# Performance work log

Hardware: AMD Instinct MI355X
Metric: run time of the kernel (lower is better)

Reference implementation:

```python
import jax, jax.numpy as jnp
import numpy as np
from jax import lax

# ---- config (matches init_kwargs) ----
B, T, H = 4, 2048, 1024
HU = 4 * H                 # h_up = hidden*4
LAYERS, INDEX = 12, 0
K_CLAMP, K_EPS = 60.0, 1e-8
LN_EPS = 1e-5


def setup_inputs() -> dict:
    key = jax.random.key(0)
    ks = jax.random.split(key, 9)
    s = 0.02  # weight scale
    tr01 = INDEX / (LAYERS - 1)          # time_ratio_0_to_1
    tr1pz = 1.0 - INDEX / LAYERS         # time_ratio_1_to_pz
    i_h = np.arange(H, dtype=np.float64) / H
    i_hu = np.arange(HU, dtype=np.float64)
    # per-channel decay speed / first (sized to the WKV channel dim h_up)
    decay_speed = -5.0 + 8.0 * (i_hu / (HU - 1)) ** (0.7 + 1.3 * tr01)
    zigzag = ((np.arange(HU) + 1) % 3 - 1) * 0.5
    time_first = np.log(0.3) + zigzag
    f32 = lambda a: jnp.asarray(a, jnp.float32)
    return {
        "x": jax.random.normal(ks[0], (B, T, H), jnp.float32),
        "ln0_g": jnp.ones((H,), jnp.float32), "ln0_b": jnp.zeros((H,), jnp.float32),
        "pre_g": jnp.ones((H,), jnp.float32), "pre_b": jnp.zeros((H,), jnp.float32),
        "post_g": jnp.ones((H,), jnp.float32), "post_b": jnp.zeros((H,), jnp.float32),
        "tm_decay": f32(decay_speed),
        "tm_first": f32(time_first),
        "tm_mix_k": f32(i_h ** tr1pz),
        "tm_mix_v": f32(i_h ** tr1pz + 0.3 * tr01),
        "tm_mix_r": f32(i_h ** (0.5 * tr1pz)),
        "tm_Wk": jax.random.normal(ks[1], (H, HU), jnp.float32) * s,
        "tm_Wv": jax.random.normal(ks[2], (H, HU), jnp.float32) * s,
        "tm_Wr": jax.random.normal(ks[3], (H, HU), jnp.float32) * s,
        "tm_Wo": jax.random.normal(ks[4], (HU, H), jnp.float32) * s,
        "cm_mix_k": f32(i_h ** tr1pz),
        "cm_mix_r": f32(i_h ** tr1pz),
        "cm_Wk": jax.random.normal(ks[5], (H, HU), jnp.float32) * s,
        "cm_Wv": jax.random.normal(ks[6], (HU, H), jnp.float32) * s,
        "cm_Wr": jax.random.normal(ks[7], (H, H), jnp.float32) * s,
    }


def _ln(x, g, b):
    m = jnp.mean(x, -1, keepdims=True)
    v = jnp.mean((x - m) ** 2, -1, keepdims=True)
    return (x - m) / jnp.sqrt(v + LN_EPS) * g + b


def _shift(x):  # ZeroPad2d((0,0,1,-1)): xx[:, t] = x[:, t-1], xx[:, 0] = 0
    return jnp.pad(x[:, :-1], ((0, 0), (1, 0), (0, 0)))


def _wkv(k, kv, decay, first):
    # k, kv: [B, T, HU]; decay, first: [HU]
    # wkv[t] = first*kv[t] + sum_{d>=1} decay^(d-1) * kv[t-d]  (same for k)
    def step(carry, inp):
        sk, skv = carry
        kt, kvt = inp
        out = (first * kt + sk, first * kvt + skv)
        return (kt + decay * sk, kvt + decay * skv), out
    b = k.shape[0]
    init = (jnp.zeros((b, k.shape[2]), k.dtype), jnp.zeros((b, k.shape[2]), k.dtype))
    _, (wk, wkv) = lax.scan(step, init, (jnp.swapaxes(k, 0, 1), jnp.swapaxes(kv, 0, 1)))
    return jnp.swapaxes(wk, 0, 1), jnp.swapaxes(wkv, 0, 1)


def reference(x, ln0_g, ln0_b, pre_g, pre_b, post_g, post_b,
              tm_decay, tm_first, tm_mix_k, tm_mix_v, tm_mix_r,
              tm_Wk, tm_Wv, tm_Wr, tm_Wo,
              cm_mix_k, cm_mix_r, cm_Wk, cm_Wv, cm_Wr):
    if INDEX == 0:
        x = _ln(x, ln0_g, ln0_b)

    # ---- RWKV_TM (time mix / WKV) ----
    xn = _ln(x, pre_g, pre_b)
    xx = _shift(xn)
    xk = xn * tm_mix_k + xx * (1.0 - tm_mix_k)
    xv = xn * tm_mix_v + xx * (1.0 - tm_mix_v)
    xr = xn * tm_mix_r + xx * (1.0 - tm_mix_r)
    k = jnp.exp(jnp.minimum(xk @ tm_Wk, K_CLAMP))   # [B,T,HU]
    v = xv @ tm_Wv                                  # [B,T,HU]
    r = xr @ tm_Wr                                  # [B,T,HU]
    kv = k * v
    decay = jnp.exp(-jnp.exp(tm_decay))  # per-step multiplier exp(-exp(time_decay))
    first = jnp.exp(tm_first)
    wk, wkv = _wkv(k, kv, decay, first)
    rwkv = jax.nn.sigmoid(r) * (wkv / (wk + K_EPS))
    x = x + rwkv @ tm_Wo

    # ---- RWKV_CM (channel mix) ----
    xn = _ln(x, post_g, post_b)
    xx = _shift(xn)
    xk = xn * cm_mix_k + xx * (1.0 - cm_mix_k)
    xr = xn * cm_mix_r + xx * (1.0 - cm_mix_r)
    kv = jax.nn.silu(xk @ cm_Wk) @ cm_Wv            # [B,T,H]
    x = x + (jax.nn.sigmoid(xr @ cm_Wr) + kv)
    return x
```

## Files before the change

### kernel.cpp

```cpp
#include <hip/hip_runtime.h>

#define Hdim  1024
#define Tdim  2048
#define Bdim  4
#define HUdim 4096
#define Mrows (Bdim*Tdim)
#define CHUNK 2048
#define NCH   (HUdim/CHUNK)
#define NSEG  16
#define SEGL  (Tdim/NSEG)
#define SCHUNK 16

typedef __bf16 bf16;
typedef __bf16 bf16x2 __attribute__((ext_vector_type(2)));
typedef __bf16 bf16x8 __attribute__((ext_vector_type(8)));
typedef float  floatx4 __attribute__((ext_vector_type(4)));

__device__ __forceinline__ bf16 f2bf(float x) { return (bf16)x; }

__global__ __launch_bounds__(256) void wconv_all(
    const float* __restrict__ s0, const float* __restrict__ s1, const float* __restrict__ s2,
    const float* __restrict__ s3, const float* __restrict__ s4, const float* __restrict__ s5,
    const float* __restrict__ s6,
    bf16* d0, bf16* d1, bf16* d2, bf16* d3, bf16* d4, bf16* d5, bf16* d6) {
  __shared__ float tile[64][65];
  int bid = blockIdx.x;
  const float* src; bf16* dst; int K, N, local;
  if (bid < 1024)      { src = s0; dst = d0; K = Hdim;  N = HUdim; local = bid; }
  else if (bid < 2048) { src = s1; dst = d1; K = Hdim;  N = HUdim; local = bid - 1024; }
  else if (bid < 3072) { src = s2; dst = d2; K = Hdim;  N = HUdim; local = bid - 2048; }
  else if (bid < 4096) { src = s3; dst = d3; K = HUdim; N = Hdim;  local = bid - 3072; }
  else if (bid < 5120) { src = s4; dst = d4; K = Hdim;  N = HUdim; local = bid - 4096; }
  else if (bid < 6144) { src = s5; dst = d5; K = HUdim; N = Hdim;  local = bid - 5120; }
  else                 { src = s6; dst = d6; K = Hdim;  N = Hdim;  local = bid - 6144; }
  const int nt = N >> 6;
  const int n0 = (local % nt) * 64, k0 = (local / nt) * 64;
  const int tr = threadIdx.x >> 6;
  const int tc = threadIdx.x & 63;
#pragma unroll
  for (int j = 0; j < 16; j++) {
    int r = j * 4 + tr;
    tile[r][tc] = src[(size_t)(k0 + r) * N + n0 + tc];
  }
  __syncthreads();
#pragma unroll
  for (int j = 0; j < 16; j++) {
    int r = j * 4 + tr;
    dst[(size_t)(n0 + r) * K + k0 + tc] = f2bf(tile[tc][r]);
  }
}

__device__ __forceinline__ void block_reduce4(float v[4], float* sm) {
#pragma unroll
  for (int off = 32; off > 0; off >>= 1) {
#pragma unroll
    for (int i = 0; i < 4; i++) v[i] += __shfl_down(v[i], off, 64);
  }
  const int w = threadIdx.x >> 6;
  if ((threadIdx.x & 63) == 0) {
#pragma unroll
    for (int i = 0; i < 4; i++) sm[w * 4 + i] = v[i];
  }
  __syncthreads();
#pragma unroll
  for (int i = 0; i < 4; i++) v[i] = sm[i] + sm[4 + i] + sm[8 + i] + sm[12 + i];
  __syncthreads();
}

__global__ __launch_bounds__(256) void ln_mix_tm(
    const float* __restrict__ x,
    const float* __restrict__ g0, const float* __restrict__ b0,
    const float* __restrict__ g1, const float* __restrict__ b1,
    const float* __restrict__ mk, const float* __restrict__ mv, const float* __restrict__ mr,
    float* __restrict__ x0, bf16* __restrict__ xk, bf16* __restrict__ xv, bf16* __restrict__ xr) {
  __shared__ float sm[16];
  const int bid = blockIdx.x;
  const int t = bid & (Tdim - 1);
  const int tid = threadIdx.x;
  const bool havep = (t > 0);
  const float hp = havep ? 1.f : 0.f;
  const float* rowc = x + (size_t)bid * Hdim;
  const float* rowp = havep ? (rowc - Hdim) : rowc;

  float c[4], p[4];
#pragma unroll
  for (int j = 0; j < 4; j++) c[j] = rowc[tid * 4 + j];
#pragma unroll
  for (int j = 0; j < 4; j++) p[j] = rowp[tid * 4 + j] * hp;

  float red[4] = {0.f, 0.f, 0.f, 0.f};
#pragma unroll
  for (int j = 0; j < 4; j++) { red[0] += c[j]; red[1] += c[j]*c[j]; red[2] += p[j]; red[3] += p[j]*p[j]; }
  block_reduce4(red, sm);
  const float inv = 1.f / Hdim;
  float mc = red[0]*inv, vc = red[1]*inv - mc*mc;
  float mp = red[2]*inv, vp = red[3]*inv - mp*mp;
  float sc = rsqrtf(vc + 1e-5f), sp = rsqrtf(vp + 1e-5f);

  float yc[4], yp[4];
#pragma unroll
  for (int j = 0; j < 4; j++) {
    int i = tid * 4 + j;
    yc[j] = (c[j] - mc) * sc * g0[i] + b0[i];
    yp[j] = ((p[j] - mp) * sp * g0[i] + b0[i]) * hp;
    x0[(size_t)bid * Hdim + i] = yc[j];
  }

  float r2[4] = {0.f, 0.f, 0.f, 0.f};
#pragma unroll
  for (int j = 0; j < 4; j++) { r2[0] += yc[j]; r2[1] += yc[j]*yc[j]; r2[2] += yp[j]; r2[3] += yp[j]*yp[j]; }
  block_reduce4(r2, sm);
  float mc2 = r2[0]*inv, vc2 = r2[1]*inv - mc2*mc2;
  float mp2 = r2[2]*inv, vp2 = r2[3]*inv - mp2*mp2;
  float sc2 = rsqrtf(vc2 + 1e-5f), sp2 = rsqrtf(vp2 + 1e-5f);

#pragma unroll
  for (int j = 0; j < 4; j++) {
    int i = tid * 4 + j;
    float xnc = (yc[j] - mc2) * sc2 * g1[i] + b1[i];
    float xnp = ((yp[j] - mp2) * sp2 * g1[i] + b1[i]) * hp;
    size_t o = (size_t)bid * Hdim + i;
    float a;
    a = mk[i]; xk[o] = f2bf(xnc * a + xnp * (1.f - a));
    a = mv[i]; xv[o] = f2bf(xnc * a + xnp * (1.f - a));
    a = mr[i]; xr[o] = f2bf(xnc * a + xnp * (1.f - a));
  }
}

__global__ __launch_bounds__(256) void ln_mix_cm(
    const float* __restrict__ xin,
    const float* __restrict__ g, const float* __restrict__ bb,
    const float* __restrict__ mk, const float* __restrict__ mr,
    bf16* __restrict__ xk, bf16* __restrict__ xr) {
  __shared__ float sm[16];
  const int bid = blockIdx.x;
  const int t = bid & (Tdim - 1);
  const int tid = threadIdx.x;
  const bool havep = (t > 0);
  const float hp = havep ? 1.f : 0.f;
  const float* rowc = xin + (size_t)bid * Hdim;
  const float* rowp = havep ? (rowc - Hdim) : rowc;

  float c[4], p[4];
#pragma unroll
  for (int j = 0; j < 4; j++) c[j] = rowc[tid * 4 + j];
#pragma unroll
  for (int j = 0; j < 4; j++) p[j] = rowp[tid * 4 + j] * hp;

  float red[4] = {0.f, 0.f, 0.f, 0.f};
#pragma unroll
  for (int j = 0; j < 4; j++) { red[0] += c[j]; red[1] += c[j]*c[j]; red[2] += p[j]; red[3] += p[j]*p[j]; }
  block_reduce4(red, sm);
  const float inv = 1.f / Hdim;
  float mc = red[0]*inv, vc = red[1]*inv - mc*mc;
  float mp = red[2]*inv, vp = red[3]*inv - mp*mp;
  float sc = rsqrtf(vc + 1e-5f), sp = rsqrtf(vp + 1e-5f);

#pragma unroll
  for (int j = 0; j < 4; j++) {
    int i = tid * 4 + j;
    float xnc = (c[j] - mc) * sc * g[i] + bb[i];
    float xnp = ((p[j] - mp) * sp * g[i] + bb[i]) * hp;
    size_t o = (size_t)bid * Hdim + i;
    float a;
    a = mk[i]; xk[o] = f2bf(xnc * a + xnp * (1.f - a));
    a = mr[i]; xr[o] = f2bf(xnc * a + xnp * (1.f - a));
  }
}

__global__ __launch_bounds__(64) void wkv_part(
    const bf16* __restrict__ Kb, const bf16* __restrict__ Vb,
    float* __restrict__ stK, float* __restrict__ stKV,
    const float* __restrict__ tdec) {
  const int seg = blockIdx.x & (NSEG - 1);
  const int rest = blockIdx.x >> 4;
  const int b = rest >> 4, g = rest & 15;
  const int c = (g << 7) + (threadIdx.x << 1);
  const float d0 = __expf(-__expf(tdec[c]));
  const float d1 = __expf(-__expf(tdec[c + 1]));
  size_t base = ((size_t)b * Tdim + (size_t)seg * SEGL) * CHUNK + c;
  float sk0 = 0.f, skv0 = 0.f, sk1 = 0.f, skv1 = 0.f;
  for (int t0 = 0; t0 < SEGL; t0 += SCHUNK) {
    bf16x2 kk[SCHUNK], vv[SCHUNK];
#pragma unroll
    for (int j = 0; j < SCHUNK; j++) {
      size_t idx = base + (size_t)(t0 + j) * CHUNK;
      kk[j] = *(const bf16x2*)(Kb + idx);
      vv[j] = *(const bf16x2*)(Vb + idx);
    }
#pragma unroll
    for (int j = 0; j < SCHUNK; j++) {
      float k0 = (float)kk[j][0], k1 = (float)kk[j][1];
      float v0 = (float)vv[j][0], v1 = (float)vv[j][1];
      sk0  = fmaf(d0, sk0, k0);   skv0 = fmaf(d0, skv0, k0 * v0);
      sk1  = fmaf(d1, sk1, k1);   skv1 = fmaf(d1, skv1, k1 * v1);
    }
  }
  size_t so = ((size_t)seg * Bdim + b) * CHUNK + c;
  stK[so]      = sk0;  stK[so + 1]  = sk1;
  stKV[so]     = skv0; stKV[so + 1] = skv1;
}

__global__ __launch_bounds__(64) void wkv_emit(
    const bf16* __restrict__ Kb, const bf16* __restrict__ Vb,
    const bf16* SRb, bf16* Pb,
    const float* __restrict__ stK, const float* __restrict__ stKV,
    const float* __restrict__ tdec, const float* __restrict__ tfst) {
  const int seg = blockIdx.x & (NSEG - 1);
  const int rest = blockIdx.x >> 4;
  const int b = rest >> 4, g = rest & 15;
  const int c = (g << 7) + (threadIdx.x << 1);
  const float ed0 = __expf(tdec[c]),     ed1 = __expf(tdec[c + 1]);
  const float d0  = __expf(-ed0),        d1  = __expf(-ed1);
  const float df0 = __expf(-ed0 * (float)SEGL);
  const float df1 = __expf(-ed1 * (float)SEGL);
  const float f0  = __expf(tfst[c]),     f1  = __expf(tfst[c + 1]);

  float sk0 = 0.f, skv0 = 0.f, sk1 = 0.f, skv1 = 0.f;
  for (int j = 0; j < seg; j++) {
    size_t so = ((size_t)j * Bdim + b) * CHUNK + c;
    sk0  = fmaf(df0, sk0,  stK[so]);      sk1  = fmaf(df1, sk1,  stK[so + 1]);
    skv0 = fmaf(df0, skv0, stKV[so]);     skv1 = fmaf(df1, skv1, stKV[so + 1]);
  }

  size_t base = ((size_t)b * Tdim + (size_t)seg * SEGL) * CHUNK + c;
  for (int t0 = 0; t0 < SEGL; t0 += SCHUNK) {
    bf16x2 kk[SCHUNK], vv[SCHUNK], rr[SCHUNK];
#pragma unroll
    for (int j = 0; j < SCHUNK; j++) {
      size_t idx = base + (size_t)(t0 + j) * CHUNK;
      kk[j] = *(const bf16x2*)(Kb + idx);
      vv[j] = *(const bf16x2*)(Vb + idx);
      rr[j] = *(const bf16x2*)(SRb + idx);
    }
#pragma unroll
    for (int j = 0; j < SCHUNK; j++) {
      size_t idx = base + (size_t)(t0 + j) * CHUNK;
      float k0 = (float)kk[j][0], k1 = (float)kk[j][1];
      float v0 = (float)vv[j][0], v1 = (float)vv[j][1];
      float kv0 = k0 * v0, kv1 = k1 * v1;
      float wk0  = fmaf(f0, k0, sk0) + 1e-8f;
      float wk1  = fmaf(f1, k1, sk1) + 1e-8f;
      float wkv0 = fmaf(f0, kv0, skv0);
      float wkv1 = fmaf(f1, kv1, skv1);
      bf16x2 out;
      out[0] = f2bf((float)rr[j][0] * wkv0 * __builtin_amdgcn_rcpf(wk0));
      out[1] = f2bf((float)rr[j][1] * wkv1 * __builtin_amdgcn_rcpf(wk1));
      *(bf16x2*)(Pb + idx) = out;
      sk0  = fmaf(d0, sk0, k0);   skv0 = fmaf(d0, skv0, kv0);
      sk1  = fmaf(d1, sk1, k1);   skv1 = fmaf(d1, skv1, kv1);
    }
  }
}

__device__ __forceinline__ void gld_lds(const bf16* g, bf16* l) {
  __builtin_amdgcn_global_load_lds(
      (const __attribute__((address_space(1))) void*)(g),
      (__attribute__((address_space(3))) void*)(l),
      16, 0, 0);
}

__device__ __forceinline__ void swz(int s, int gm, int& m_t, int& n_t) {
  const int mpx  = gm >> 3;
  const int xcd  = s & 7;
  const int ss   = s >> 3;
  const int pass = mpx << 1;
  const int ng   = ss / pass;
  const int rem  = ss - ng * pass;
  m_t = xcd * mpx + (rem >> 1);
  n_t = (ng << 1) + (rem & 1);
}

enum { E_EXP = 0, E_BF16 = 1, E_SIG = 2, E_ADD1 = 3, E_SILU = 4, E_F32 = 5, E_SIGADD2 = 6 };

template <int EPI>
__device__ __forceinline__ void epilogue(
    floatx4 acc[4][4], void* Cout, const void* aux1, const void* aux2,
    long m0, long n0, int ldc, int lane, int wm, int wn) {
  const int r0 = wm * 64 + ((lane >> 4) << 2);
  const int c0 = wn * 64 + (lane & 15);
#pragma unroll
  for (int mt = 0; mt < 4; mt++) {
#pragma unroll
    for (int i = 0; i < 4; i++) {
      long r = m0 + r0 + mt * 16 + i;
      long bidx = r * (long)ldc + n0 + c0;
#pragma unroll
      for (int nt = 0; nt < 4; nt++) {
        long idx = bidx + nt * 16;
        float v = acc[mt][nt][i];
        if constexpr (EPI == E_EXP) {
          ((bf16*)Cout)[idx] = f2bf(__expf(fminf(v, 60.f)));
        } else if constexpr (EPI == E_BF16) {
          ((bf16*)Cout)[idx] = f2bf(v);
        } else if constexpr (EPI == E_SIG) {
          ((bf16*)Cout)[idx] = f2bf(1.f / (1.f + __expf(-v)));
        } else if constexpr (EPI == E_ADD1) {
          float prev = ((const float*)aux1)[idx];
          ((float*)Cout)[idx] = v + prev;
        } else if constexpr (EPI == E_SILU) {
          ((bf16*)Cout)[idx] = f2bf(v / (1.f + __expf(-v)));
        } else if constexpr (EPI == E_F32) {
          ((float*)Cout)[idx] = v;
        } else {
          float a1 = ((const float*)aux1)[idx];
          float a2 = ((const float*)aux2)[idx];
          ((float*)Cout)[idx] = a1 + 1.f / (1.f + __expf(-v)) + a2;
        }
      }
    }
  }
}

__device__ __forceinline__ void mm_core_n128(
    const bf16* __restrict__ A, const bf16* __restrict__ Bt,
    int lda, int ldb, int K, long m0, long n0,
    int wv, int lane, bf16* Lds, floatx4 acc[4][4]) {
  const int rl  = lane >> 2;
  const int scol = (((lane & 3) - ((lane >> 3) & 3)) & 3) * 8;
  const bf16* gA = A + (m0 + wv * 16 + rl) * (long)lda + scol;
  const bf16* gB = Bt + (n0 + wv * 16 + rl) * (long)ldb + scol;
  bf16* lA = Lds + wv * 512;
  bf16* lB = Lds + 49152 + wv * 512;

  const int wm = wv >> 1, wn = wv & 1;
  const int pg = ((lane >> 4) + ((lane >> 1) & 3)) & 3;
  const bf16* fa0 = Lds + (wm * 64 + (lane & 15)) * 32 + pg * 8;
  const bf16* fb0 = Lds + 49152 + (wn * 64 + (lane & 15)) * 32 + pg * 8;

#define STGA_N(buf, h, kt) do { \
    const bf16* _s = gA + (long)(h) * 128 * lda + (long)(kt) * 64; \
    bf16* _d = lA + (buf) * 16384 + (h) * 4096; \
    gld_lds(_s, _d); gld_lds(_s + 32, _d + 8192); } while (0)
#define STGB_N(buf, kt) do { \
    const bf16* _s = gB + (long)(kt) * 64; \
    bf16* _d = lB + (buf) * 8192; \
    gld_lds(_s, _d); gld_lds(_s + 32, _d + 4096); } while (0)

  STGA_N(0, 0, 0); STGA_N(0, 1, 0); STGB_N(0, 0);
  STGA_N(1, 0, 1); STGA_N(1, 1, 1); STGB_N(1, 1);
  asm volatile("s_waitcnt vmcnt(6)" ::: "memory");
  __builtin_amdgcn_s_barrier();

  const int niter = K >> 6;
  int p = 0;
  for (int it = 0; it < niter; ++it) {
    const int q = (p >= 1) ? p - 1 : p + 2;
    const bool dostage = (it <= niter - 3);
    const bf16* fa = fa0 + p * 16384;
    const bf16* fb = fb0 + p * 8192;

    bf16x8 a0[4], b0v[4];
#pragma unroll
    for (int i = 0; i < 4; ++i) {
      a0[i]  = *(const bf16x8*)(fa + i * 512);
      b0v[i] = *(const bf16x8*)(fb + i * 512);
    }
    __builtin_amdgcn_sched_barrier(0);
    if (dostage) { STGA_N(q, 0, it + 2); STGA_N(q, 1, it + 2); }
    asm volatile("s_waitcnt lgkmcnt(0)" ::: "memory");
    __builtin_amdgcn_s_setprio(1);
#pragma unroll
    for (int mf = 0; mf < 4; ++mf)
#pragma unroll
      for (int nf = 0; nf < 4; ++nf)
        acc[mf][nf] = __builtin_amdgcn_mfma_f32_16x16x32_bf16(a0[mf], b0v[nf], acc[mf][nf], 0, 0, 0);
    __builtin_amdgcn_s_setprio(0);

    bf16x8 a1[4], b1v[4];
#pragma unroll
    for (int i = 0; i < 4; ++i) {
      a1[i]  = *(const bf16x8*)(fa + 8192 + i * 512);
      b1v[i] = *(const bf16x8*)(fb + 4096 + i * 512);
    }
    __builtin_amdgcn_sched_barrier(0);
    if (dostage) STGB_N(q, it + 2);
    asm volatile("s_waitcnt lgkmcnt(0)" ::: "memory");
    __builtin_amdgcn_s_setprio(1);
#pragma unroll
    for (int mf = 0; mf < 4; ++mf)
#pragma unroll
      for (int nf = 0; nf < 4; ++nf)
        acc[mf][nf] = __builtin_amdgcn_mfma_f32_16x16x32_bf16(a1[mf], b1v[nf], acc[mf][nf], 0, 0, 0);
    __builtin_amdgcn_s_setprio(0);

    if (it < niter - 1) {
      if (dostage) asm volatile("s_waitcnt vmcnt(6)" ::: "memory");
      else         asm volatile("s_waitcnt vmcnt(0)" ::: "memory");
      __builtin_amdgcn_s_barrier();
    }
    p = (p == 2) ? 0 : p + 1;
  }
#undef STGA_N
#undef STGB_N
}

template <int EPI>
__global__ __launch_bounds__(512, 2) void gemm8n(
    const bf16* __restrict__ A, const bf16* __restrict__ Bt,
    void* Cout, const void* aux1, const void* aux2,
    int lda, int ldb, int ldc, int K, int gm, int gn) {
  __shared__ __align__(16) bf16 Lds[73728];
  const int tid = threadIdx.x;
  const int lane = tid & 63;
  const int wv = tid >> 6;
  int m_t, n_t;
  swz(blockIdx.x, gm, m_t, n_t);
  const long m0 = (long)m_t * 256, n0 = (long)n_t * 128;
  floatx4 acc[4][4];
#pragma unroll
  for (int i = 0; i < 4; i++)
#pragma unroll
    for (int j = 0; j < 4; j++) acc[i][j] = (floatx4){0.f, 0.f, 0.f, 0.f};
  mm_core_n128(A, Bt, lda, ldb, K, m0, n0, wv, lane, Lds, acc);
  const int wm = wv >> 1, wn = wv & 1;
  epilogue<EPI>(acc, Cout, aux1, aux2, m0, n0, ldc, lane, wm, wn);
}

__device__ __forceinline__ void mm_core256(
    const bf16* __restrict__ A, const bf16* __restrict__ Bt,
    int lda, int ldb, int K, long m0, long n0,
    int wv, int lane, bf16* Lds, floatx4 acc[8][4]) {
  const int wm = wv >> 2, wn = wv & 3;
  const int rA0 = wm * 128 + (wv & 3) * 16;
  const int rB0 = (wv >> 1) * 64 + (wv & 1) * 16;
  const int rl  = lane >> 2;
  const int scol = (((lane & 3) - ((lane >> 3) & 3)) & 3) * 8;
  const bf16* gA = A + (m0 + rA0 + rl) * (long)lda + scol;
  const bf16* gB = Bt + (n0 + rB0 + rl) * (long)ldb + scol;
  bf16* lA = Lds + rA0 * 32;
  bf16* lB = Lds + 16384 + rB0 * 32;

  const int pg = ((lane >> 4) + ((lane >> 1) & 3)) & 3;
  const bf16* fa0 = Lds + (wm * 128 + (lane & 15)) * 32 + pg * 8;
  const bf16* fb0 = Lds + 16384 + (wn * 64 + (lane & 15)) * 32 + pg * 8;

#define STGA8(buf, h, kt) do { \
    const bf16* _s = gA + (long)(h) * 64 * lda + (kt) * 64; \
    bf16* _d = lA + (buf) * 32768 + (h) * 2048; \
    gld_lds(_s, _d); gld_lds(_s + 32, _d + 8192); } while (0)
#define STGB8(buf, h, kt) do { \
    const bf16* _s = gB + (long)(h) * 32 * ldb + (kt) * 64; \
    bf16* _d = lB + (buf) * 32768 + (h) * 1024; \
    gld_lds(_s, _d); gld_lds(_s + 32, _d + 8192); } while (0)

  STGA8(0, 0, 0); STGB8(0, 0, 0); STGB8(0, 1, 0); STGA8(0, 1, 0);
  STGA8(1, 0, 1); STGB8(1, 0, 1); STGB8(1, 1, 1);
  asm volatile("s_waitcnt vmcnt(10)" ::: "memory");
  __builtin_amdgcn_s_barrier();

  const int niter = K >> 7;
  bf16x8 a[4][2];
  bf16x8 b[2][2][2];
  for (int it = 0; it < niter; ++it) {
    const int kt0 = it << 1;
    const bool notlast = (it != niter - 1);
#pragma unroll
    for (int ph = 0; ph < 8; ++ph) {
      const int q   = ph & 3;
      const int buf = ph >> 2;
      const int mq  = q >> 1;
      const int nq  = (q >> 1) ^ (q & 1);
      const bf16* fa = fa0 + buf * 32768 + mq * 2048;
      const bf16* fb = fb0 + buf * 32768 + nq * 1024;
      if (q == 0) {
#pragma unroll
        for (int mf = 0; mf < 4; ++mf) {
          a[mf][0] = *(const bf16x8*)(fa + mf * 512);
          a[mf][1] = *(const bf16x8*)(fa + mf * 512 + 8192);
        }
#pragma unroll
        for (int nf = 0; nf < 2; ++nf) {
          b[0][nf][0] = *(const bf16x8*)(fb + nf * 512);
          b[0][nf][1] = *(const bf16x8*)(fb + nf * 512 + 8192);
        }
      } else if (q == 1) {
#pragma unroll
        for (int nf = 0; nf < 2; ++nf) {
          b[1][nf][0] = *(const bf16x8*)(fb + nf * 512);
          b[1][nf][1] = *(const bf16x8*)(fb + nf * 512 + 8192);
        }
      } else if (q == 2) {
#pragma unroll
        for (int mf = 0; mf < 4; ++mf) {
          a[mf][0] = *(const bf16x8*)(fa + mf * 512);
          a[mf][1] = *(const bf16x8*)(fa + mf * 512 + 8192);
        }
      }
      __builtin_amdgcn_sched_barrier(0);
      if (ph == 0)            STGA8(1, 1, kt0 + 1);
      else if (notlast) {
        if (ph == 1)      STGA8(0, 0, kt0 + 2);
        else if (ph == 2) STGB8(0, 0, kt0 + 2);
        else if (ph == 3) STGB8(0, 1, kt0 + 2);
        else if (ph == 4) STGA8(0, 1, kt0 + 2);
        else if (ph == 5) STGA8(1, 0, kt0 + 3);
        else if (ph == 6) STGB8(1, 0, kt0 + 3);
        else              STGB8(1, 1, kt0 + 3);
      }
      if (notlast) {
        if (ph == 0 || ph == 1 || ph == 4 || ph == 5)
          asm volatile("s_waitcnt vmcnt(10)" ::: "memory");
        else if (ph == 3 || ph == 7)
          asm volatile("s_waitcnt vmcnt(12)" ::: "memory");
      } else {
        if (ph == 0)      asm volatile("s_waitcnt vmcnt(10)" ::: "memory");
        else if (ph == 1) asm volatile("s_waitcnt vmcnt(0)" ::: "memory");
      }
      if (q != 3) {
        __builtin_amdgcn_s_barrier();
        asm volatile("s_waitcnt lgkmcnt(0)" ::: "memory");
      }
      __builtin_amdgcn_s_setprio(1);
#pragma unroll
      for (int mf = 0; mf < 4; ++mf)
#pragma unroll
        for (int nf = 0; nf < 2; ++nf) {
          acc[mq*4+mf][nq*2+nf] = __builtin_amdgcn_mfma_f32_16x16x32_bf16(
              a[mf][0], b[nq][nf][0], acc[mq*4+mf][nq*2+nf], 0, 0, 0);
          acc[mq*4+mf][nq*2+nf] = __builtin_amdgcn_mfma_f32_16x16x32_bf16(
              a[mf][1], b[nq][nf][1], acc[mq*4+mf][nq*2+nf], 0, 0, 0);
        }
      __builtin_amdgcn_s_setprio(0);
      __builtin_amdgcn_s_barrier();
    }
  }
#undef STGA8
#undef STGB8
}

template <int EPI>
__global__ __launch_bounds__(512, 2) void gemm8(
    const bf16* __restrict__ A, const bf16* __restrict__ Bt,
    void* Cout, const void* aux1, const void* aux2,
    int lda, int ldb, int ldc, int K, int gm, int gn) {
  __shared__ __align__(16) bf16 Lds[65536];
  const int tid = threadIdx.x;
  const int lane = tid & 63;
  const int wv = tid >> 6;
  int m_t, n_t;
  swz(blockIdx.x, gm, m_t, n_t);
  const long m0 = (long)m_t * 256, n0 = (long)n_t * 256;
  floatx4 acc[8][4];
#pragma unroll
  for (int i = 0; i < 8; i++)
#pragma unroll
    for (int j = 0; j < 4; j++) acc[i][j] = (floatx4){0.f, 0.f, 0.f, 0.f};
  mm_core256(A, Bt, lda, ldb, K, m0, n0, wv, lane, Lds, acc);

  const int wm = wv >> 2, wn = wv & 3;
  const int r0 = wm * 128 + ((lane >> 4) << 2);
  const int c0 = wn * 64 + (lane & 15);
#pragma unroll
  for (int mf = 0; mf < 8; ++mf) {
#pragma unroll
    for (int i = 0; i < 4; ++i) {
      long r = m0 + r0 + mf * 16 + i;
      long bidx = r * (long)ldc + n0 + c0;
#pragma unroll
      for (int nf = 0; nf < 4; ++nf) {
        long idx = bidx + nf * 16;
        float v = acc[mf][nf][i];
        if constexpr (EPI == E_SILU) {
          ((bf16*)Cout)[idx] = f2bf(v / (1.f + __expf(-v)));
        } else if constexpr (EPI == E_BF16) {
          ((bf16*)Cout)[idx] = f2bf(v);
        } else if constexpr (EPI == E_F32) {
          ((float*)Cout)[idx] = v;
        } else if constexpr (EPI == E_ADD1) {
          float prev = ((const float*)aux1)[idx];
          ((float*)Cout)[idx] = v + prev;
        }
      }
    }
  }
}

__global__ __launch_bounds__(512, 2) void proj8(
    const bf16* __restrict__ xk, const bf16* __restrict__ xv, const bf16* __restrict__ xr,
    const bf16* __restrict__ Wk, const bf16* __restrict__ Wv, const bf16* __restrict__ Wr,
    bf16* Kc, bf16* Vc, bf16* SRc, int gm, int gn) {
  __shared__ __align__(16) bf16 Lds[65536];
  const int per = gm * gn;
  const int sub = blockIdx.x / per;
  const int s   = blockIdx.x - sub * per;
  const int tid = threadIdx.x;
  const int lane = tid & 63;
  const int wv = tid >> 6;
  int m_t, n_t;
  swz(s, gm, m_t, n_t);
  const long m0 = (long)m_t * 256, n0 = (long)n_t * 256;

  const bf16* A  = (sub == 0) ? xk : (sub == 1) ? xv : xr;
  const bf16* Bt = (sub == 0) ? Wk : (sub == 1) ? Wv : Wr;
  bf16*       C  = (sub == 0) ? Kc : (sub == 1) ? Vc : SRc;

  floatx4 acc[8][4];
#pragma unroll
  for (int i = 0; i < 8; i++)
#pragma unroll
    for (int j = 0; j < 4; j++) acc[i][j] = (floatx4){0.f, 0.f, 0.f, 0.f};
  mm_core256(A, Bt, Hdim, Hdim, Hdim, m0, n0, wv, lane, Lds, acc);

  const int wm = wv >> 2, wn = wv & 3;
  const int r0 = wm * 128 + ((lane >> 4) << 2);
  const int c0 = wn * 64 + (lane & 15);
#pragma unroll
  for (int mf = 0; mf < 8; ++mf) {
#pragma unroll
    for (int i = 0; i < 4; ++i) {
      long r = m0 + r0 + mf * 16 + i;
      long bidx = r * (long)CHUNK + n0 + c0;
#pragma unroll
      for (int nf = 0; nf < 4; ++nf) {
        long idx = bidx + nf * 16;
        float v = acc[mf][nf][i];
        float o;
        if (sub == 0)      o = __expf(fminf(v, 60.f));
        else if (sub == 1) o = v;
        else               o = 1.f / (1.f + __expf(-v));
        C[idx] = f2bf(o);
      }
    }
  }
}

extern "C" void kernel_launch(void* const* d_in, const int* in_sizes, int n_in,
                              void* d_out, int out_size, void* d_ws, size_t ws_size,
                              hipStream_t stream) {
  (void)in_sizes; (void)n_in; (void)out_size; (void)ws_size;
  const float* x        = (const float*)d_in[0];
  const float* ln0_g    = (const float*)d_in[1];
  const float* ln0_b    = (const float*)d_in[2];
  const float* pre_g    = (const float*)d_in[3];
  const float* pre_b    = (const float*)d_in[4];
  const float* post_g   = (const float*)d_in[5];
  const float* post_b   = (const float*)d_in[6];
  const float* tm_decay = (const float*)d_in[7];
  const float* tm_first = (const float*)d_in[8];
  const float* tm_mix_k = (const float*)d_in[9];
  const float* tm_mix_v = (const float*)d_in[10];
  const float* tm_mix_r = (const float*)d_in[11];
  const float* tm_Wk    = (const float*)d_in[12];
  const float* tm_Wv    = (const float*)d_in[13];
  const float* tm_Wr    = (const float*)d_in[14];
  const float* tm_Wo    = (const float*)d_in[15];
  const float* cm_mix_k = (const float*)d_in[16];
  const float* cm_mix_r = (const float*)d_in[17];
  const float* cm_Wk    = (const float*)d_in[18];
  const float* cm_Wv    = (const float*)d_in[19];
  const float* cm_Wr    = (const float*)d_in[20];

  char* ws = (char*)d_ws;
  bf16*  WkT  = (bf16*)(ws + 0);
  bf16*  WvT  = (bf16*)(ws + 8388608);
  bf16*  WrT  = (bf16*)(ws + 16777216);
  bf16*  WoT  = (bf16*)(ws + 25165824);
  bf16*  cWkT = (bf16*)(ws + 33554432);
  bf16*  cWvT = (bf16*)(ws + 41943040);
  bf16*  cWrT = (bf16*)(ws + 50331648);
  float* xres = (float*)(ws + 52428800);
  bf16*  xk   = (bf16*)(ws + 85983232);
  bf16*  xv   = (bf16*)(ws + 102760448);
  bf16*  xr   = (bf16*)(ws + 119537664);
  bf16*  Kc   = (bf16*)(ws + 136314880);
  bf16*  Vc   = (bf16*)(ws + 169869312);
  bf16*  SRc  = (bf16*)(ws + 203423744);
  float* stK  = (float*)(ws + 236978176);
  float* stKV = (float*)(ws + 237502464);
  bf16*  xk2  = (bf16*)(ws + 136314880);
  bf16*  xr2  = (bf16*)(ws + 153092096);
  bf16*  hbuf = (bf16*)(ws + 169869312);
  float* hv   = (float*)(ws + 85983232);

  dim3 blk(256);
  wconv_all<<<6400, blk, 0, stream>>>(tm_Wk, tm_Wv, tm_Wr, tm_Wo, cm_Wk, cm_Wv, cm_Wr,
                                      WkT, WvT, WrT, WoT, cWkT, cWvT, cWrT);

  ln_mix_tm<<<Mrows, blk, 0, stream>>>(x, ln0_g, ln0_b, pre_g, pre_b,
                                       tm_mix_k, tm_mix_v, tm_mix_r, xres, xk, xv, xr);

  const int scan_grid = NSEG * Bdim * (CHUNK / 128);
  const int GM8 = Mrows / 256;
  const int GN8p = CHUNK / 256;
  const int GNn = Hdim / 128;
  for (int ch = 0; ch < NCH; ch++) {
    const long woff = (long)ch * CHUNK;
    proj8<<<3 * GM8 * GN8p, dim3(512), 0, stream>>>(
        xk, xv, xr, WkT + woff * Hdim, WvT + woff * Hdim, WrT + woff * Hdim,
        Kc, Vc, SRc, GM8, GN8p);

    wkv_part<<<scan_grid, dim3(64), 0, stream>>>(
        Kc, Vc, stK, stKV, tm_decay + woff);
    wkv_emit<<<scan_grid, dim3(64), 0, stream>>>(
        Kc, Vc, SRc, SRc, stK, stKV, tm_decay + woff, tm_first + woff);

    gemm8n<E_ADD1><<<GM8 * GNn, dim3(512), 0, stream>>>(
        SRc, WoT + woff, xres, xres, nullptr, CHUNK, HUdim, Hdim, CHUNK, GM8, GNn);
  }

  ln_mix_cm<<<Mrows, blk, 0, stream>>>(xres, post_g, post_b, cm_mix_k, cm_mix_r, xk2, xr2);

  gemm8<E_SILU><<<GM8 * (HUdim/256), dim3(512), 0, stream>>>(
      xk2, cWkT, hbuf, nullptr, nullptr, Hdim, Hdim, HUdim, Hdim, GM8, HUdim/256);

  gemm8n<E_F32><<<GM8 * GNn, dim3(512), 0, stream>>>(
      hbuf, cWvT, hv, nullptr, nullptr, HUdim, HUdim, Hdim, HUdim, GM8, GNn);

  gemm8n<E_SIGADD2><<<GM8 * GNn, dim3(512), 0, stream>>>(
      xr2, cWrT, (float*)d_out, xres, hv, Hdim, Hdim, Hdim, Hdim, GM8, GNn);
}
```

Measured before the change: 867.5 us.

## Make projection and SiLU GEMMs persistent over multiple tiles with prologue overlap

```diff
diff --git a/kernel.cpp b/kernel.cpp
--- a/kernel.cpp
+++ b/kernel.cpp
@@ -417,38 +417,26 @@
   epilogue<EPI>(acc, Cout, aux1, aux2, m0, n0, ldc, lane, wm, wn);
 }
 
-__device__ __forceinline__ void mm_core256(
-    const bf16* __restrict__ A, const bf16* __restrict__ Bt,
-    int lda, int ldb, int K, long m0, long n0,
-    int wv, int lane, bf16* Lds, floatx4 acc[8][4]) {
-  const int wm = wv >> 2, wn = wv & 3;
-  const int rA0 = wm * 128 + (wv & 3) * 16;
-  const int rB0 = (wv >> 1) * 64 + (wv & 1) * 16;
-  const int rl  = lane >> 2;
-  const int scol = (((lane & 3) - ((lane >> 3) & 3)) & 3) * 8;
-  const bf16* gA = A + (m0 + rA0 + rl) * (long)lda + scol;
-  const bf16* gB = Bt + (n0 + rB0 + rl) * (long)ldb + scol;
-  bf16* lA = Lds + rA0 * 32;
-  bf16* lB = Lds + 16384 + rB0 * 32;
-
-  const int pg = ((lane >> 4) + ((lane >> 1) & 3)) & 3;
-  const bf16* fa0 = Lds + (wm * 128 + (lane & 15)) * 32 + pg * 8;
-  const bf16* fb0 = Lds + 16384 + (wn * 64 + (lane & 15)) * 32 + pg * 8;
-
-#define STGA8(buf, h, kt) do { \
-    const bf16* _s = gA + (long)(h) * 64 * lda + (kt) * 64; \
-    bf16* _d = lA + (buf) * 32768 + (h) * 2048; \
-    gld_lds(_s, _d); gld_lds(_s + 32, _d + 8192); } while (0)
-#define STGB8(buf, h, kt) do { \
-    const bf16* _s = gB + (long)(h) * 32 * ldb + (kt) * 64; \
-    bf16* _d = lB + (buf) * 32768 + (h) * 1024; \
-    gld_lds(_s, _d); gld_lds(_s + 32, _d + 8192); } while (0)
-
-  STGA8(0, 0, 0); STGB8(0, 0, 0); STGB8(0, 1, 0); STGA8(0, 1, 0);
-  STGA8(1, 0, 1); STGB8(1, 0, 1); STGB8(1, 1, 1);
-  asm volatile("s_waitcnt vmcnt(10)" ::: "memory");
-  __builtin_amdgcn_s_barrier();
-
+__device__ __forceinline__ void stgA8(const bf16* gA, bf16* lA, int lda, int buf, int h, int kt) {
+  const bf16* s = gA + (long)h * 64 * lda + kt * 64;
+  bf16* d = lA + buf * 32768 + h * 2048;
+  gld_lds(s, d); gld_lds(s + 32, d + 8192);
+}
+__device__ __forceinline__ void stgB8(const bf16* gB, bf16* lB, int ldb, int buf, int h, int kt) {
+  const bf16* s = gB + (long)h * 32 * ldb + kt * 64;
+  bf16* d = lB + buf * 32768 + h * 1024;
+  gld_lds(s, d); gld_lds(s + 32, d + 8192);
+}
+__device__ __forceinline__ void stage_pro256(const bf16* gA, const bf16* gB, int lda, int ldb,
+                                             bf16* lA, bf16* lB) {
+  stgA8(gA, lA, lda, 0, 0, 0); stgB8(gB, lB, ldb, 0, 0, 0);
+  stgB8(gB, lB, ldb, 0, 1, 0); stgA8(gA, lA, lda, 0, 1, 0);
+  stgA8(gA, lA, lda, 1, 0, 1); stgB8(gB, lB, ldb, 1, 0, 1); stgB8(gB, lB, ldb, 1, 1, 1);
+}
+
+__device__ __forceinline__ void core256_loop(
+    const bf16* gA, const bf16* gB, int lda, int ldb, int K,
+    const bf16* fa0, const bf16* fb0, bf16* lA, bf16* lB, floatx4 acc[8][4]) {
   const int niter = K >> 7;
   bf16x8 a[4][2];
   bf16x8 b[2][2][2];
@@ -488,15 +476,15 @@
         }
       }
       __builtin_amdgcn_sched_barrier(0);
-      if (ph == 0)            STGA8(1, 1, kt0 + 1);
+      if (ph == 0)            stgA8(gA, lA, lda, 1, 1, kt0 + 1);
       else if (notlast) {
-        if (ph == 1)      STGA8(0, 0, kt0 + 2);
-        else if (ph == 2) STGB8(0, 0, kt0 + 2);
-        else if (ph == 3) STGB8(0, 1, kt0 + 2);
-        else if (ph == 4) STGA8(0, 1, kt0 + 2);
-        else if (ph == 5) STGA8(1, 0, kt0 + 3);
-        else if (ph == 6) STGB8(1, 0, kt0 + 3);
-        else              STGB8(1, 1, kt0 + 3);
+        if (ph == 1)      stgA8(gA, lA, lda, 0, 0, kt0 + 2);
+        else if (ph == 2) stgB8(gB, lB, ldb, 0, 0, kt0 + 2);
+        else if (ph == 3) stgB8(gB, lB, ldb, 0, 1, kt0 + 2);
+        else if (ph == 4) stgA8(gA, lA, lda, 0, 1, kt0 + 2);
+        else if (ph == 5) stgA8(gA, lA, lda, 1, 0, kt0 + 3);
+        else if (ph == 6) stgB8(gB, lB, ldb, 1, 0, kt0 + 3);
+        else              stgB8(gB, lB, ldb, 1, 1, kt0 + 3);
       }
       if (notlast) {
         if (ph == 0 || ph == 1 || ph == 4 || ph == 5)
@@ -525,15 +513,12 @@
       __builtin_amdgcn_s_barrier();
     }
   }
-#undef STGA8
-#undef STGB8
-}
-
-template <int EPI>
-__global__ __launch_bounds__(512, 2) void gemm8(
-    const bf16* __restrict__ A, const bf16* __restrict__ Bt,
-    void* Cout, const void* aux1, const void* aux2,
-    int lda, int ldb, int ldc, int K, int gm, int gn) {
+}
+
+__global__ __launch_bounds__(512, 2) void proj8p(
+    const bf16* __restrict__ xk, const bf16* __restrict__ xv, const bf16* __restrict__ xr,
+    const bf16* __restrict__ Wk, const bf16* __restrict__ Wv, const bf16* __restrict__ Wr,
+    bf16* Kc, bf16* Vc, bf16* SRc, int gm, int gn) {
   __shared__ __align__(16) bf16 Lds[65536];
   const int tid = threadIdx.x;
   const int lane = tid & 63;
@@ -541,86 +526,139 @@
   int m_t, n_t;
   swz(blockIdx.x, gm, m_t, n_t);
   const long m0 = (long)m_t * 256, n0 = (long)n_t * 256;
-  floatx4 acc[8][4];
-#pragma unroll
-  for (int i = 0; i < 8; i++)
-#pragma unroll
-    for (int j = 0; j < 4; j++) acc[i][j] = (floatx4){0.f, 0.f, 0.f, 0.f};
-  mm_core256(A, Bt, lda, ldb, K, m0, n0, wv, lane, Lds, acc);
-
   const int wm = wv >> 2, wn = wv & 3;
+  const int rA0 = wm * 128 + (wv & 3) * 16;
+  const int rB0 = (wv >> 1) * 64 + (wv & 1) * 16;
+  const int rl  = lane >> 2;
+  const int scol = (((lane & 3) - ((lane >> 3) & 3)) & 3) * 8;
+  bf16* lA = Lds + rA0 * 32;
+  bf16* lB = Lds + 16384 + rB0 * 32;
+  const int pg = ((lane >> 4) + ((lane >> 1) & 3)) & 3;
+  const bf16* fa0 = Lds + (wm * 128 + (lane & 15)) * 32 + pg * 8;
+  const bf16* fb0 = Lds + 16384 + (wn * 64 + (lane & 15)) * 32 + pg * 8;
+
+  const long aoff = (m0 + rA0 + rl) * (long)Hdim + scol;
+  const long boff = (n0 + rB0 + rl) * (long)Hdim + scol;
+  const bf16* gA0 = xk + aoff;  const bf16* gB0 = Wk + boff;
+  const bf16* gA1 = xv + aoff;  const bf16* gB1 = Wv + boff;
+  const bf16* gA2 = xr + aoff;  const bf16* gB2 = Wr + boff;
+
+  stage_pro256(gA0, gB0, Hdim, Hdim, lA, lB);
+  asm volatile("s_waitcnt vmcnt(10)" ::: "memory");
+  __builtin_amdgcn_s_barrier();
+
   const int r0 = wm * 128 + ((lane >> 4) << 2);
   const int c0 = wn * 64 + (lane & 15);
-#pragma unroll
-  for (int mf = 0; mf < 8; ++mf) {
-#pragma unroll
-    for (int i = 0; i < 4; ++i) {
-      long r = m0 + r0 + mf * 16 + i;
-      long bidx = r * (long)ldc + n0 + c0;
-#pragma unroll
-      for (int nf = 0; nf < 4; ++nf) {
-        long idx = bidx + nf * 16;
-        float v = acc[mf][nf][i];
-        if constexpr (EPI == E_SILU) {
-          ((bf16*)Cout)[idx] = f2bf(v / (1.f + __expf(-v)));
-        } else if constexpr (EPI == E_BF16) {
-          ((bf16*)Cout)[idx] = f2bf(v);
-        } else if constexpr (EPI == E_F32) {
-          ((float*)Cout)[idx] = v;
-        } else if constexpr (EPI == E_ADD1) {
-          float prev = ((const float*)aux1)[idx];
-          ((float*)Cout)[idx] = v + prev;
+
+#pragma unroll 1
+  for (int sub = 0; sub < 3; ++sub) {
+    const bf16* gA = (sub == 0) ? gA0 : (sub == 1) ? gA1 : gA2;
+    const bf16* gB = (sub == 0) ? gB0 : (sub == 1) ? gB1 : gB2;
+    floatx4 acc[8][4];
+#pragma unroll
+    for (int i = 0; i < 8; i++)
+#pragma unroll
+      for (int j = 0; j < 4; j++) acc[i][j] = (floatx4){0.f, 0.f, 0.f, 0.f};
+    core256_loop(gA, gB, Hdim, Hdim, Hdim, fa0, fb0, lA, lB, acc);
+
+    if (sub == 0)      stage_pro256(gA1, gB1, Hdim, Hdim, lA, lB);
+    else if (sub == 1) stage_pro256(gA2, gB2, Hdim, Hdim, lA, lB);
+
+    bf16* C = (sub == 0) ? Kc : (sub == 1) ? Vc : SRc;
+#pragma unroll
+    for (int mf = 0; mf < 8; ++mf) {
+#pragma unroll
+      for (int i = 0; i < 4; ++i) {
+        long r = m0 + r0 + mf * 16 + i;
+        long bidx = r * (long)CHUNK + n0 + c0;
+#pragma unroll
+        for (int nf = 0; nf < 4; ++nf) {
+          float v = acc[mf][nf][i];
+          float o = (sub == 0) ? __expf(fminf(v, 60.f))
+                  : (sub == 1) ? v
+                  : 1.f / (1.f + __expf(-v));
+          C[bidx + nf * 16] = f2bf(o);
         }
       }
     }
-  }
-}
-
-__global__ __launch_bounds__(512, 2) void proj8(
-    const bf16* __restrict__ xk, const bf16* __restrict__ xv, const bf16* __restrict__ xr,
-    const bf16* __restrict__ Wk, const bf16* __restrict__ Wv, const bf16* __restrict__ Wr,
-    bf16* Kc, bf16* Vc, bf16* SRc, int gm, int gn) {
+    if (sub < 2) {
+      asm volatile("s_waitcnt vmcnt(10)" ::: "memory");
+      __builtin_amdgcn_s_barrier();
+    }
+  }
+}
+
+template <int EPI>
+__global__ __launch_bounds__(512, 2) void gemm8p2(
+    const bf16* __restrict__ A, const bf16* __restrict__ Bt,
+    void* Cout, int lda, int ldb, int ldc, int K, int gm, int gn) {
   __shared__ __align__(16) bf16 Lds[65536];
-  const int per = gm * gn;
-  const int sub = blockIdx.x / per;
-  const int s   = blockIdx.x - sub * per;
   const int tid = threadIdx.x;
   const int lane = tid & 63;
   const int wv = tid >> 6;
-  int m_t, n_t;
-  swz(s, gm, m_t, n_t);
-  const long m0 = (long)m_t * 256, n0 = (long)n_t * 256;
-
-  const bf16* A  = (sub == 0) ? xk : (sub == 1) ? xv : xr;
-  const bf16* Bt = (sub == 0) ? Wk : (sub == 1) ? Wv : Wr;
-  bf16*       C  = (sub == 0) ? Kc : (sub == 1) ? Vc : SRc;
-
-  floatx4 acc[8][4];
-#pragma unroll
-  for (int i = 0; i < 8; i++)
-#pragma unroll
-    for (int j = 0; j < 4; j++) acc[i][j] = (floatx4){0.f, 0.f, 0.f, 0.f};
-  mm_core256(A, Bt, Hdim, Hdim, Hdim, m0, n0, wv, lane, Lds, acc);
-
+  int mt0, nt0, mt1, nt1;
+  swz(blockIdx.x, gm, mt0, nt0);
+  swz(blockIdx.x + (int)gridDim.x, gm, mt1, nt1);
+  const long m0_0 = (long)mt0 * 256, n0_0 = (long)nt0 * 256;
+  const long m0_1 = (long)mt1 * 256, n0_1 = (long)nt1 * 256;
   const int wm = wv >> 2, wn = wv & 3;
+  const int rA0 = wm * 128 + (wv & 3) * 16;
+  const int rB0 = (wv >> 1) * 64 + (wv & 1) * 16;
+  const int rl  = lane >> 2;
+  const int scol = (((lane & 3) - ((lane >> 3) & 3)) & 3) * 8;
+  bf16* lA = Lds + rA0 * 32;
+  bf16* lB = Lds + 16384 + rB0 * 32;
+  const int pg = ((lane >> 4) + ((lane >> 1) & 3)) & 3;
+  const bf16* fa0 = Lds + (wm * 128 + (lane & 15)) * 32 + pg * 8;
+  const bf16* fb0 = Lds + 16384 + (wn * 64 + (lane & 15)) * 32 + pg * 8;
+
+  const bf16* gA_0 = A  + (m0_0 + rA0 + rl) * (long)lda + scol;
+  const bf16* gB_0 = Bt + (n0_0 + rB0 + rl) * (long)ldb + scol;
+  const bf16* gA_1 = A  + (m0_1 + rA0 + rl) * (long)lda + scol;
+  const bf16* gB_1 = Bt + (n0_1 + rB0 + rl) * (long)ldb + scol;
+
+  stage_pro256(gA_0, gB_0, lda, ldb, lA, lB);
+  asm volatile("s_waitcnt vmcnt(10)" ::: "memory");
+  __builtin_amdgcn_s_barrier();
+
   const int r0 = wm * 128 + ((lane >> 4) << 2);
   const int c0 = wn * 64 + (lane & 15);
-#pragma unroll
-  for (int mf = 0; mf < 8; ++mf) {
-#pragma unroll
-    for (int i = 0; i < 4; ++i) {
-      long r = m0 + r0 + mf * 16 + i;
-      long bidx = r * (long)CHUNK + n0 + c0;
-#pragma unroll
-      for (int nf = 0; nf < 4; ++nf) {
-        long idx = bidx + nf * 16;
-        float v = acc[mf][nf][i];
-        float o;
-        if (sub == 0)      o = __expf(fminf(v, 60.f));
-        else if (sub == 1) o = v;
-        else               o = 1.f / (1.f + __expf(-v));
-        C[idx] = f2bf(o);
+
+#pragma unroll 1
+  for (int t = 0; t < 2; ++t) {
+    const bf16* gA = (t == 0) ? gA_0 : gA_1;
+    const bf16* gB = (t == 0) ? gB_0 : gB_1;
+    const long m0 = (t == 0) ? m0_0 : m0_1;
+    const long n0 = (t == 0) ? n0_0 : n0_1;
+    floatx4 acc[8][4];
+#pragma unroll
+    for (int i = 0; i < 8; i++)
+#pragma unroll
+      for (int j = 0; j < 4; j++) acc[i][j] = (floatx4){0.f, 0.f, 0.f, 0.f};
+    core256_loop(gA, gB, lda, ldb, K, fa0, fb0, lA, lB, acc);
+
+    if (t == 0) stage_pro256(gA_1, gB_1, lda, ldb, lA, lB);
+
+#pragma unroll
+    for (int mf = 0; mf < 8; ++mf) {
+#pragma unroll
+      for (int i = 0; i < 4; ++i) {
+        long r = m0 + r0 + mf * 16 + i;
+        long bidx = r * (long)ldc + n0 + c0;
+#pragma unroll
+        for (int nf = 0; nf < 4; ++nf) {
+          float v = acc[mf][nf][i];
+          if constexpr (EPI == E_SILU) {
+            ((bf16*)Cout)[bidx + nf * 16] = f2bf(v / (1.f + __expf(-v)));
+          } else {
+            ((bf16*)Cout)[bidx + nf * 16] = f2bf(v);
+          }
+        }
       }
+    }
+    if (t == 0) {
+      asm volatile("s_waitcnt vmcnt(10)" ::: "memory");
+      __builtin_amdgcn_s_barrier();
     }
   }
 }
@@ -686,7 +724,7 @@
   const int GNn = Hdim / 128;
   for (int ch = 0; ch < NCH; ch++) {
     const long woff = (long)ch * CHUNK;
-    proj8<<<3 * GM8 * GN8p, dim3(512), 0, stream>>>(
+    proj8p<<<GM8 * GN8p, dim3(512), 0, stream>>>(
         xk, xv, xr, WkT + woff * Hdim, WvT + woff * Hdim, WrT + woff * Hdim,
         Kc, Vc, SRc, GM8, GN8p);
 
@@ -701,8 +739,8 @@
 
   ln_mix_cm<<<Mrows, blk, 0, stream>>>(xres, post_g, post_b, cm_mix_k, cm_mix_r, xk2, xr2);
 
-  gemm8<E_SILU><<<GM8 * (HUdim/256), dim3(512), 0, stream>>>(
-      xk2, cWkT, hbuf, nullptr, nullptr, Hdim, Hdim, HUdim, Hdim, GM8, HUdim/256);
+  gemm8p2<E_SILU><<<(GM8 * (HUdim/256)) / 2, dim3(512), 0, stream>>>(
+      xk2, cWkT, hbuf, Hdim, Hdim, HUdim, Hdim, GM8, HUdim/256);
 
   gemm8n<E_F32><<<GM8 * GNn, dim3(512), 0, stream>>>(
       hbuf, cWvT, hv, nullptr, nullptr, HUdim, HUdim, Hdim, HUdim, GM8, GNn);
```

After: 1.071 ms. 23.5% more time.
